# Kernel optimization log

Hardware: AMD Instinct MI355X
Metric: run time of the kernel (lower is better)

## Reference

```python
import jax, jax.numpy as jnp
import numpy as np

WINDOW = 7
NUM_HEADS = 16
HEAD_DIM = 32  # dim=512 / 16 heads
SCALE = HEAD_DIM ** -0.5


def _relative_position_index(ws: int) -> np.ndarray:
    ch, cw = np.meshgrid(np.arange(ws), np.arange(ws), indexing='ij')
    coords = np.stack([ch, cw]).reshape(2, -1)            # [2, ws*ws]
    rel = coords[:, :, None] - coords[:, None, :]          # [2, N, N]
    rel = rel.transpose(1, 2, 0)                           # [N, N, 2]
    rel[:, :, 0] += ws - 1
    rel[:, :, 1] += ws - 1
    rel[:, :, 0] *= 2 * ws - 1
    return rel.sum(-1)                                     # [N, N]

REL_IDX = jnp.asarray(_relative_position_index(WINDOW))   # [49, 49] int


def setup_inputs() -> dict:
    key = jax.random.key(0)
    ks = jax.random.split(key, 6)
    B, N, C = 2048, WINDOW * WINDOW, NUM_HEADS * HEAD_DIM
    return {
        'hidden_states': jax.random.normal(ks[0], (B, N, C), jnp.float32),
        'attention_mask': jnp.zeros((B, N, N), jnp.float32),
        'qkv_w': jax.random.normal(ks[1], (3 * C, C), jnp.float32) * 0.02,
        'qkv_b': jax.random.normal(ks[2], (3 * C,), jnp.float32) * 0.02,
        'out_w': jax.random.normal(ks[3], (C, C), jnp.float32) * 0.02,
        'out_b': jax.random.normal(ks[4], (C,), jnp.float32) * 0.02,
        'rel_pos_table': jax.random.normal(ks[5], ((2 * WINDOW - 1) ** 2, NUM_HEADS), jnp.float32) * 0.02,
    }


def reference(hidden_states, attention_mask, qkv_w, qkv_b, out_w, out_b, rel_pos_table):
    B, N, C = hidden_states.shape
    H, D = NUM_HEADS, HEAD_DIM
    qkv = hidden_states @ qkv_w.T + qkv_b                  # [B, N, 3C]
    q, k, v = jnp.split(qkv, 3, axis=-1)
    q = q.reshape(B, N, H, D).transpose(0, 2, 1, 3)        # [B, H, N, D]
    k = k.reshape(B, N, H, D).transpose(0, 2, 1, 3)
    v = v.reshape(B, N, H, D).transpose(0, 2, 1, 3)
    attn = jnp.einsum('bhnd,bhmd->bhnm', q, k) * SCALE     # [B, H, N, N]
    # relative position bias: gather [N*N] rows -> [N, N, H] -> [1, H, N, N]
    bias = rel_pos_table[REL_IDX.reshape(-1)].reshape(N, N, H).transpose(2, 0, 1)
    attn = attn + bias[None] + attention_mask[:, None]
    attn = jax.nn.softmax(attn, axis=-1)                   # dropout = identity (eval)
    out = jnp.einsum('bhnm,bhmd->bhnd', attn, v)           # [B, H, N, D]
    out = out.transpose(0, 2, 1, 3).reshape(B, N, C)
    return out @ out_w.T + out_b
```

## Files before the change

kernel.cpp:

```cpp
#include <hip/hip_runtime.h>
#include <hip/hip_bf16.h>

typedef __attribute__((ext_vector_type(8))) __bf16 bf16x8;
typedef __attribute__((ext_vector_type(4))) __bf16 bf16x4;
typedef __attribute__((ext_vector_type(4))) float f32x4;

#define MFMA16(a,b,c) __builtin_amdgcn_mfma_f32_16x16x32_bf16(a,b,c,0,0,0)

__device__ __forceinline__ void gload_lds16(const void* g, void* l) {
  __builtin_amdgcn_global_load_lds(
      (const __attribute__((address_space(1))) void*)g,
      (__attribute__((address_space(3))) void*)l, 16, 0, 0);
}

__device__ __forceinline__ f32x4 max4(f32x4 a, f32x4 b) {
  f32x4 c;
  c[0] = fmaxf(a[0], b[0]); c[1] = fmaxf(a[1], b[1]);
  c[2] = fmaxf(a[2], b[2]); c[3] = fmaxf(a[3], b[3]);
  return c;
}

__global__ void prep_k(const float* __restrict__ qkv_w, const float* __restrict__ out_w,
                       const float* __restrict__ rpt,
                       __bf16* __restrict__ qwb, __bf16* __restrict__ owb,
                       __bf16* __restrict__ biasb)
{
  int i = blockIdx.x * 256 + threadIdx.x;
  if (i < 786432) { qwb[i] = (__bf16)qkv_w[i]; return; }
  i -= 786432;
  if (i < 262144) { owb[i] = (__bf16)out_w[i]; return; }
  i -= 262144;
  if (i < 65536) {
    int hh = i >> 12, qc = i & 4095, qq = qc >> 6, c = qc & 63;
    __bf16 val;
    if (c >= 49)      val = (__bf16)(-30000.0f);
    else if (qq >= 49) val = (__bf16)(0.0f);
    else {
      int dh = qq / 7 - c / 7 + 6;
      int dw = qq % 7 - c % 7 + 6;
      val = (__bf16)rpt[(dh * 13 + dw) * 16 + hh];
    }
    biasb[i] = val;
  }
}

__global__ void cast_k(const float* __restrict__ in, __bf16* __restrict__ outb, int n8)
{
  int i = blockIdx.x * blockDim.x + threadIdx.x;
  int stride = gridDim.x * blockDim.x;
  for (; i < n8; i += stride) {
    const float4* p = (const float4*)in + (size_t)i * 2;
    float4 x = p[0], y = p[1];
    bf16x8 o;
    o[0] = (__bf16)x.x; o[1] = (__bf16)x.y; o[2] = (__bf16)x.z; o[3] = (__bf16)x.w;
    o[4] = (__bf16)y.x; o[5] = (__bf16)y.y; o[6] = (__bf16)y.z; o[7] = (__bf16)y.w;
    ((bf16x8*)outb)[i] = o;
  }
}

template<int EPI>
__global__ __launch_bounds__(512, 2)
void gemm8p(const __bf16* __restrict__ A, const __bf16* __restrict__ Bt,
            const float* __restrict__ bvec, float* __restrict__ outp,
            __bf16* __restrict__ qb, __bf16* __restrict__ kb, __bf16* __restrict__ vb,
            int N, int K)
{
  __shared__ __align__(16) char lds[131072];
  const int tid = threadIdx.x;
  const int wave = tid >> 6, lane = tid & 63;
  const int g = lane >> 4, r = lane & 15;
  const int l8 = lane >> 3, l7 = lane & 7;

  const int ntiles = N >> 8;
  const int nper = gridDim.x >> 3;
  const int b2 = (blockIdx.x & 7) * nper + (blockIdx.x >> 3);
  const int m0 = (b2 / ntiles) << 8;
  const int n0 = (b2 % ntiles) << 8;

  const __bf16* Ag = A + (size_t)(m0 + wave * 8 + l8) * K + (l7 ^ l8) * 8;
  const __bf16* Bg = Bt + (size_t)(n0 + wave * 8 + l8) * K + (l7 ^ l8) * 8;
  const size_t c64 = (size_t)64 * K;

  const int ch0 = (g ^ (r & 7)) << 4;
  const int ch1 = ((4 + g) ^ (r & 7)) << 4;
  const char* Ar = lds + ((wave >> 2) * 128 + r) * 128;
  const char* Br = lds + 32768 + ((wave & 3) * 64 + r) * 128;

  f32x4 acc[8][4] = {};
  bf16x8 a[4][2], b[4][2];

#pragma unroll
  for (int c = 0; c < 4; ++c) {
    gload_lds16(Ag + c * c64, lds + wave * 1024 + c * 8192);
    gload_lds16(Bg + c * c64, lds + 32768 + wave * 1024 + c * 8192);
  }
#pragma unroll
  for (int c = 0; c < 4; ++c) {
    gload_lds16(Ag + 64 + c * c64, lds + 65536 + wave * 1024 + c * 8192);
    gload_lds16(Bg + 64 + c * c64, lds + 65536 + 32768 + wave * 1024 + c * 8192);
  }

#pragma unroll 1
  for (int kt = 0; kt < 8; ++kt) {
    const int cur = (kt & 1) << 16;
    const char* Ab = Ar + cur;
    const char* Bb = Br + cur;
    if (kt == 7) asm volatile("s_waitcnt vmcnt(0)" ::: "memory");
    else         asm volatile("s_waitcnt vmcnt(8)" ::: "memory");
    __builtin_amdgcn_s_barrier();

#pragma unroll
    for (int mi = 0; mi < 4; ++mi) {
      a[mi][0] = *(const bf16x8*)(Ab + mi * 2048 + ch0);
      a[mi][1] = *(const bf16x8*)(Ab + mi * 2048 + ch1);
    }
#pragma unroll
    for (int ni = 0; ni < 2; ++ni) {
      b[ni][0] = *(const bf16x8*)(Bb + ni * 2048 + ch0);
      b[ni][1] = *(const bf16x8*)(Bb + ni * 2048 + ch1);
    }
    __builtin_amdgcn_s_barrier();
    asm volatile("s_waitcnt lgkmcnt(0)" ::: "memory");
    __builtin_amdgcn_s_setprio(1);
#pragma unroll
    for (int mi = 0; mi < 4; ++mi)
#pragma unroll
      for (int ni = 0; ni < 2; ++ni) {
        acc[mi][ni] = MFMA16(a[mi][0], b[ni][0], acc[mi][ni]);
        acc[mi][ni] = MFMA16(a[mi][1], b[ni][1], acc[mi][ni]);
      }
    __builtin_amdgcn_s_setprio(0);
    __builtin_amdgcn_s_barrier();

#pragma unroll
    for (int ni = 2; ni < 4; ++ni) {
      b[ni][0] = *(const bf16x8*)(Bb + ni * 2048 + ch0);
      b[ni][1] = *(const bf16x8*)(Bb + ni * 2048 + ch1);
    }
    __builtin_amdgcn_s_barrier();
    asm volatile("s_waitcnt lgkmcnt(0)" ::: "memory");
    __builtin_amdgcn_s_setprio(1);
#pragma unroll
    for (int mi = 0; mi < 4; ++mi)
#pragma unroll
      for (int ni = 2; ni < 4; ++ni) {
        acc[mi][ni] = MFMA16(a[mi][0], b[ni][0], acc[mi][ni]);
        acc[mi][ni] = MFMA16(a[mi][1], b[ni][1], acc[mi][ni]);
      }
    __builtin_amdgcn_s_setprio(0);
    __builtin_amdgcn_s_barrier();

#pragma unroll
    for (int mi = 0; mi < 4; ++mi) {
      a[mi][0] = *(const bf16x8*)(Ab + (4 + mi) * 2048 + ch0);
      a[mi][1] = *(const bf16x8*)(Ab + (4 + mi) * 2048 + ch1);
    }
    __builtin_amdgcn_s_barrier();
    asm volatile("s_waitcnt lgkmcnt(0)" ::: "memory");
    __builtin_amdgcn_s_setprio(1);
#pragma unroll
    for (int mi = 0; mi < 4; ++mi)
#pragma unroll
      for (int ni = 2; ni < 4; ++ni) {
        acc[4 + mi][ni] = MFMA16(a[mi][0], b[ni][0], acc[4 + mi][ni]);
        acc[4 + mi][ni] = MFMA16(a[mi][1], b[ni][1], acc[4 + mi][ni]);
      }
    __builtin_amdgcn_s_setprio(0);
    __builtin_amdgcn_s_barrier();

    if (kt < 6) {
      const __bf16* Agk = Ag + (kt + 2) * 64;
      const __bf16* Bgk = Bg + (kt + 2) * 64;
      char* Al = lds + cur + wave * 1024;
      char* Bl = lds + cur + 32768 + wave * 1024;
#pragma unroll
      for (int c = 0; c < 4; ++c) {
        gload_lds16(Agk + c * c64, Al + c * 8192);
        gload_lds16(Bgk + c * c64, Bl + c * 8192);
      }
    }
    __builtin_amdgcn_s_setprio(1);
#pragma unroll
    for (int mi = 0; mi < 4; ++mi)
#pragma unroll
      for (int ni = 0; ni < 2; ++ni) {
        acc[4 + mi][ni] = MFMA16(a[mi][0], b[ni][0], acc[4 + mi][ni]);
        acc[4 + mi][ni] = MFMA16(a[mi][1], b[ni][1], acc[4 + mi][ni]);
      }
    __builtin_amdgcn_s_setprio(0);
    __builtin_amdgcn_s_barrier();
  }

  if (EPI == 1) {
#pragma unroll
    for (int mi = 0; mi < 8; ++mi) {
      int row = m0 + (wave >> 2) * 128 + mi * 16 + g * 4;
#pragma unroll
      for (int ni = 0; ni < 4; ++ni) {
        int col = n0 + (wave & 3) * 64 + ni * 16 + r;
        float bv = bvec[col];
#pragma unroll
        for (int j = 0; j < 4; ++j)
          outp[(size_t)(row + j) * N + col] = acc[mi][ni][j] + bv;
      }
    }
  } else {
    __bf16* dst; float scl;
    const int which = n0 >> 9;
    if (which == 0)      { dst = qb; scl = 0.17677669529663687f; }
    else if (which == 1) { dst = kb; scl = 1.0f; }
    else                 { dst = vb; scl = 1.0f; }
    float bv[4];
#pragma unroll
    for (int ni = 0; ni < 4; ++ni) bv[ni] = bvec[n0 + (wave & 3) * 64 + ni * 16 + r];
#pragma unroll
    for (int mi = 0; mi < 8; ++mi) {
#pragma unroll
      for (int j = 0; j < 4; ++j) {
        int m = m0 + (wave >> 2) * 128 + mi * 16 + g * 4 + j;
        int bb = m / 49, t = m - bb * 49;
        __bf16* drow = dst + ((size_t)bb * 16) * 1568 + t * 32;
#pragma unroll
        for (int ni = 0; ni < 4; ++ni) {
          int nl = (n0 + (wave & 3) * 64 + ni * 16 + r) & 511;
          int hh = nl >> 5, d = nl & 31;
          float val = (acc[mi][ni][j] + bv[ni]) * scl;
          drow[(size_t)hh * 1568 + d] = (__bf16)val;
        }
      }
    }
  }
}

__global__ __launch_bounds__(256, 4)
void attn_k(const __bf16* __restrict__ qb, const __bf16* __restrict__ kb,
            const __bf16* __restrict__ vb, const __bf16* __restrict__ bias_p,
            const float* __restrict__ mask, __bf16* __restrict__ ao)
{
  __shared__ float maskl[64 * 64];
  __shared__ __bf16 Vt[4][32 * 64];
  __shared__ __bf16 Pl[4][16 * 64];
  const int tid = threadIdx.x, wave = tid >> 6, lane = tid & 63;
  const int g = lane >> 4, r = lane & 15;
  const int b = blockIdx.x >> 2, hg = blockIdx.x & 3;
  const int h = hg * 4 + wave;
  const size_t bh = (size_t)b * 16 + h;
  const __bf16* q = qb + bh * 1568;
  const __bf16* k = kb + bh * 1568;
  const __bf16* v = vb + bh * 1568;
  const bf16x8 z8 = {};
  const f32x4 z4 = {};

  bf16x4 bfr[4][4];
  {
    const __bf16* bp = bias_p + h * 4096;
#pragma unroll
    for (int qi = 0; qi < 4; ++qi)
#pragma unroll
      for (int mi = 0; mi < 4; ++mi)
        bfr[qi][mi] = *(const bf16x4*)(bp + (qi * 16 + r) * 64 + mi * 16 + g * 4);
  }

  bf16x8* vtz = (bf16x8*)Vt[wave];
#pragma unroll
  for (int i = 0; i < 4; ++i) vtz[i * 64 + lane] = z8;

  const float* mb = mask + (size_t)b * 2401;
#pragma unroll
  for (int i = 0; i < 16; ++i) {
    int idx = i * 256 + tid;
    int qq = idx >> 6, c = idx & 63;
    float mv = (qq < 49 && c < 49) ? mb[qq * 49 + c] : 0.0f;
    maskl[qq * 64 + (c ^ ((qq & 7) << 2))] = mv;
  }

  bf16x8 kf[4], qf[4];
#pragma unroll
  for (int i = 0; i < 4; ++i) {
    int row = i * 16 + r;
    kf[i] = (row < 49) ? *(const bf16x8*)(k + row * 32 + g * 8) : z8;
    qf[i] = (row < 49) ? *(const bf16x8*)(q + row * 32 + g * 8) : z8;
  }

  __syncthreads();

  char* vt = (char*)Vt[wave];
#pragma unroll
  for (int i = 0; i < 4; ++i) {
    int idx = i * 64 + lane;
    int t = idx >> 2, d0 = (idx & 3) << 3;
    if (t < 49) {
      bf16x8 vv = *(const bf16x8*)(v + t * 32 + d0);
#pragma unroll
      for (int j = 0; j < 8; ++j) {
        int d = d0 + j;
        *(__bf16*)(vt + d * 128 + ((t * 2) ^ ((d & 7) << 4))) = vv[j];
      }
    }
  }

  bf16x8 vf[2][2];
#pragma unroll
  for (int di = 0; di < 2; ++di) {
    int row = di * 16 + r;
#pragma unroll
    for (int t = 0; t < 2; ++t)
      vf[di][t] = *(const bf16x8*)(vt + row * 128 + (((t * 32 + g * 8) * 2) ^ ((row & 7) << 4)));
  }

  char* pw = (char*)Pl[wave];
  __bf16* aob = ao + (size_t)b * 25088 + h * 32;
  const int swz = (r & 7) << 4;
  const int mswz = (r & 7) << 2;

#pragma unroll
  for (int qi = 0; qi < 4; ++qi) {
    f32x4 s[4];
#pragma unroll
    for (int mi = 0; mi < 4; ++mi) s[mi] = MFMA16(kf[mi], qf[qi], z4);

    const int qrow = qi * 16 + r;
#pragma unroll
    for (int mi = 0; mi < 4; ++mi) {
      int c0 = mi * 16 + g * 4;
      f32x4 m4 = *(const f32x4*)(maskl + qrow * 64 + (c0 ^ mswz));
#pragma unroll
      for (int jj = 0; jj < 4; ++jj)
        s[mi][jj] += (float)bfr[qi][mi][jj] + m4[jj];
    }
    f32x4 aa = max4(max4(s[0], s[1]), max4(s[2], s[3]));
    float mx = fmaxf(fmaxf(aa[0], aa[1]), fmaxf(aa[2], aa[3]));
    mx = fmaxf(mx, __shfl_xor(mx, 16));
    mx = fmaxf(mx, __shfl_xor(mx, 32));
    float sum = 0.0f;
#pragma unroll
    for (int mi = 0; mi < 4; ++mi) {
#pragma unroll
      for (int jj = 0; jj < 4; ++jj) {
        float e = __expf(s[mi][jj] - mx);
        s[mi][jj] = e;
        sum += e;
      }
    }
    sum += __shfl_xor(sum, 16);
    sum += __shfl_xor(sum, 32);
    const float rinv = 1.0f / sum;

#pragma unroll
    for (int mi = 0; mi < 4; ++mi) {
      bf16x4 w;
#pragma unroll
      for (int jj = 0; jj < 4; ++jj) w[jj] = (__bf16)(s[mi][jj] * rinv);
      *(bf16x4*)(pw + r * 128 + (((mi * 16 + g * 4) * 2) ^ swz)) = w;
    }
    bf16x8 pa0 = *(const bf16x8*)(pw + r * 128 + ((g * 16) ^ swz));
    bf16x8 pa1 = *(const bf16x8*)(pw + r * 128 + ((64 + g * 16) ^ swz));

#pragma unroll
    for (int di = 0; di < 2; ++di) {
      f32x4 o = MFMA16(pa0, vf[di][0], z4);
      o = MFMA16(pa1, vf[di][1], o);
#pragma unroll
      for (int jj = 0; jj < 4; ++jj) {
        int qq = qi * 16 + g * 4 + jj;
        if (qq < 49)
          aob[(size_t)qq * 512 + di * 16 + r] = (__bf16)o[jj];
      }
    }
  }
}

extern "C" void kernel_launch(void* const* d_in, const int* in_sizes, int n_in,
                              void* d_out, int out_size, void* d_ws, size_t ws_size,
                              hipStream_t stream)
{
  const float* hs    = (const float*)d_in[0];
  const float* mask  = (const float*)d_in[1];
  const float* qkv_w = (const float*)d_in[2];
  const float* qkv_b = (const float*)d_in[3];
  const float* out_w = (const float*)d_in[4];
  const float* out_b = (const float*)d_in[5];
  const float* rpt   = (const float*)d_in[6];
  float* out = (float*)d_out;

  char* ws = (char*)d_ws;
  __bf16* hsb  = (__bf16*)(ws);
  __bf16* qb   = (__bf16*)(ws + 102760448);
  __bf16* kb   = (__bf16*)(ws + 205520896);
  __bf16* vb   = (__bf16*)(ws + 308281344);
  __bf16* qwb  = (__bf16*)(ws + 411041792);
  __bf16* owb  = (__bf16*)(ws + 412614656);
  __bf16* biasb= (__bf16*)(ws + 413138944);

  prep_k<<<4352, 256, 0, stream>>>(qkv_w, out_w, rpt, qwb, owb, biasb);
  cast_k<<<2048, 256, 0, stream>>>(hs, hsb, 6422528);
  gemm8p<0><<<2352, 512, 0, stream>>>(hsb, qwb, qkv_b, nullptr, qb, kb, vb,
                                      1536, 512);
  attn_k<<<8192, 256, 0, stream>>>(qb, kb, vb, biasb, mask, hsb);
  gemm8p<1><<<784, 512, 0, stream>>>(hsb, owb, out_b, out, nullptr, nullptr, nullptr,
                                     512, 512);
}
```

Before: 540.2 us.

## Fuse fp32-to-bf16 input cast into QKV GEMM A-tile loading

Removes the separate cast kernel and instead has the QKV GEMM load fp32 hidden states through registers, convert them to bf16, and write them swizzled into LDS, while B still uses direct global-to-LDS loads. This avoids writing and re-reading an intermediate bf16 copy of the activations. In exchange, the GEMM reads twice the bytes for A on every N-tile and uses synchronous vmcnt(0) waits that may weaken the load/compute overlap. The attention kernel also now loads bias fragments inside the loop instead of holding them all in registers, which lowers register pressure.

Result: slower. 555.4 us (+2.8%).

```diff
diff --git a/kernel.cpp b/kernel.cpp
--- a/kernel.cpp
+++ b/kernel.cpp
@@ -44,23 +44,9 @@
   }
 }
 
-__global__ void cast_k(const float* __restrict__ in, __bf16* __restrict__ outb, int n8)
-{
-  int i = blockIdx.x * blockDim.x + threadIdx.x;
-  int stride = gridDim.x * blockDim.x;
-  for (; i < n8; i += stride) {
-    const float4* p = (const float4*)in + (size_t)i * 2;
-    float4 x = p[0], y = p[1];
-    bf16x8 o;
-    o[0] = (__bf16)x.x; o[1] = (__bf16)x.y; o[2] = (__bf16)x.z; o[3] = (__bf16)x.w;
-    o[4] = (__bf16)y.x; o[5] = (__bf16)y.y; o[6] = (__bf16)y.z; o[7] = (__bf16)y.w;
-    ((bf16x8*)outb)[i] = o;
-  }
-}
-
-template<int EPI>
+template<int EPI, int CVT>
 __global__ __launch_bounds__(512, 2)
-void gemm8p(const __bf16* __restrict__ A, const __bf16* __restrict__ Bt,
+void gemm8p(const void* __restrict__ Aptr, const __bf16* __restrict__ Bt,
             const float* __restrict__ bvec, float* __restrict__ outp,
             __bf16* __restrict__ qb, __bf16* __restrict__ kb, __bf16* __restrict__ vb,
             int N, int K)
@@ -77,9 +63,14 @@
   const int m0 = (b2 / ntiles) << 8;
   const int n0 = (b2 % ntiles) << 8;
 
-  const __bf16* Ag = A + (size_t)(m0 + wave * 8 + l8) * K + (l7 ^ l8) * 8;
+  const __bf16* Ab16 = (const __bf16*)Aptr;
+  const float*  Af32 = (const float*)Aptr;
+  const __bf16* Ag = Ab16 + (size_t)(m0 + wave * 8 + l8) * K + (l7 ^ l8) * 8;
   const __bf16* Bg = Bt + (size_t)(n0 + wave * 8 + l8) * K + (l7 ^ l8) * 8;
   const size_t c64 = (size_t)64 * K;
+
+  const int rowg = tid >> 4, q = tid & 15;
+  f32x4 aF[8];
 
   const int ch0 = (g ^ (r & 7)) << 4;
   const int ch1 = ((4 + g) ^ (r & 7)) << 4;
@@ -89,15 +80,44 @@
   f32x4 acc[8][4] = {};
   bf16x8 a[4][2], b[4][2];
 
-#pragma unroll
-  for (int c = 0; c < 4; ++c) {
-    gload_lds16(Ag + c * c64, lds + wave * 1024 + c * 8192);
-    gload_lds16(Bg + c * c64, lds + 32768 + wave * 1024 + c * 8192);
-  }
-#pragma unroll
-  for (int c = 0; c < 4; ++c) {
-    gload_lds16(Ag + 64 + c * c64, lds + 65536 + wave * 1024 + c * 8192);
-    gload_lds16(Bg + 64 + c * c64, lds + 65536 + 32768 + wave * 1024 + c * 8192);
+#define STAGEB_(T) {                                                           \
+    const __bf16* Bs_ = Bg + (T) * 64;                                         \
+    char* Bl_ = lds + (((T) & 1) << 16) + 32768 + wave * 1024;                 \
+    _Pragma("unroll")                                                          \
+    for (int c = 0; c < 4; ++c) gload_lds16(Bs_ + c * c64, Bl_ + c * 8192); }
+#define LOADA_F32_(T) {                                                        \
+    _Pragma("unroll")                                                          \
+    for (int j = 0; j < 8; ++j) {                                              \
+      int row_ = rowg + j * 32;                                                \
+      aF[j] = *(const f32x4*)(Af32 + (size_t)(m0 + row_) * 512 + (T) * 64 + q * 4); } }
+#define WRITEA_(T) {                                                           \
+    char* dA_ = lds + (((T) & 1) << 16);                                       \
+    _Pragma("unroll")                                                          \
+    for (int j = 0; j < 8; ++j) {                                              \
+      int row_ = rowg + j * 32;                                                \
+      bf16x4 w_;                                                               \
+      w_[0] = (__bf16)aF[j][0]; w_[1] = (__bf16)aF[j][1];                      \
+      w_[2] = (__bf16)aF[j][2]; w_[3] = (__bf16)aF[j][3];                      \
+      *(bf16x4*)(dA_ + row_ * 128 + (((q >> 1) ^ (row_ & 7)) << 4) + ((q & 1) << 3)) = w_; } }
+
+  if (CVT) {
+    STAGEB_(0); STAGEB_(1);
+    LOADA_F32_(0);
+    asm volatile("s_waitcnt vmcnt(0)" ::: "memory");
+    WRITEA_(0);
+    LOADA_F32_(1);
+    asm volatile("s_waitcnt lgkmcnt(0)" ::: "memory");
+  } else {
+#pragma unroll
+    for (int c = 0; c < 4; ++c) {
+      gload_lds16(Ag + c * c64, lds + wave * 1024 + c * 8192);
+      gload_lds16(Bg + c * c64, lds + 32768 + wave * 1024 + c * 8192);
+    }
+#pragma unroll
+    for (int c = 0; c < 4; ++c) {
+      gload_lds16(Ag + 64 + c * c64, lds + 65536 + wave * 1024 + c * 8192);
+      gload_lds16(Bg + 64 + c * c64, lds + 65536 + 32768 + wave * 1024 + c * 8192);
+    }
   }
 
 #pragma unroll 1
@@ -105,8 +125,10 @@
     const int cur = (kt & 1) << 16;
     const char* Ab = Ar + cur;
     const char* Bb = Br + cur;
-    if (kt == 7) asm volatile("s_waitcnt vmcnt(0)" ::: "memory");
-    else         asm volatile("s_waitcnt vmcnt(8)" ::: "memory");
+    if (!CVT) {
+      if (kt == 7) asm volatile("s_waitcnt vmcnt(0)" ::: "memory");
+      else         asm volatile("s_waitcnt vmcnt(8)" ::: "memory");
+    }
     __builtin_amdgcn_s_barrier();
 
 #pragma unroll
@@ -119,6 +141,7 @@
       b[ni][0] = *(const bf16x8*)(Bb + ni * 2048 + ch0);
       b[ni][1] = *(const bf16x8*)(Bb + ni * 2048 + ch1);
     }
+    if (CVT && kt >= 1 && kt < 7) LOADA_F32_(kt + 1);
     __builtin_amdgcn_s_barrier();
     asm volatile("s_waitcnt lgkmcnt(0)" ::: "memory");
     __builtin_amdgcn_s_setprio(1);
@@ -168,15 +191,23 @@
     __builtin_amdgcn_s_setprio(0);
     __builtin_amdgcn_s_barrier();
 
-    if (kt < 6) {
-      const __bf16* Agk = Ag + (kt + 2) * 64;
-      const __bf16* Bgk = Bg + (kt + 2) * 64;
-      char* Al = lds + cur + wave * 1024;
-      char* Bl = lds + cur + 32768 + wave * 1024;
-#pragma unroll
-      for (int c = 0; c < 4; ++c) {
-        gload_lds16(Agk + c * c64, Al + c * 8192);
-        gload_lds16(Bgk + c * c64, Bl + c * 8192);
+    if (CVT) {
+      if (kt < 7) {
+        asm volatile("s_waitcnt vmcnt(0)" ::: "memory");
+        WRITEA_(kt + 1);
+      }
+      if (kt < 6) STAGEB_(kt + 2);
+    } else {
+      if (kt < 6) {
+        const __bf16* Agk = Ag + (kt + 2) * 64;
+        const __bf16* Bgk = Bg + (kt + 2) * 64;
+        char* Al = lds + cur + wave * 1024;
+        char* Bl = lds + cur + 32768 + wave * 1024;
+#pragma unroll
+        for (int c = 0; c < 4; ++c) {
+          gload_lds16(Agk + c * c64, Al + c * 8192);
+          gload_lds16(Bgk + c * c64, Bl + c * 8192);
+        }
       }
     }
     __builtin_amdgcn_s_setprio(1);
@@ -188,8 +219,12 @@
         acc[4 + mi][ni] = MFMA16(a[mi][1], b[ni][1], acc[4 + mi][ni]);
       }
     __builtin_amdgcn_s_setprio(0);
-    __builtin_amdgcn_s_barrier();
-  }
+    if (CVT) asm volatile("s_waitcnt lgkmcnt(0)" ::: "memory");
+    __builtin_amdgcn_s_barrier();
+  }
+#undef STAGEB_
+#undef LOADA_F32_
+#undef WRITEA_
 
   if (EPI == 1) {
 #pragma unroll
@@ -251,16 +286,6 @@
   const bf16x8 z8 = {};
   const f32x4 z4 = {};
 
-  bf16x4 bfr[4][4];
-  {
-    const __bf16* bp = bias_p + h * 4096;
-#pragma unroll
-    for (int qi = 0; qi < 4; ++qi)
-#pragma unroll
-      for (int mi = 0; mi < 4; ++mi)
-        bfr[qi][mi] = *(const bf16x4*)(bp + (qi * 16 + r) * 64 + mi * 16 + g * 4);
-  }
-
   bf16x8* vtz = (bf16x8*)Vt[wave];
 #pragma unroll
   for (int i = 0; i < 4; ++i) vtz[i * 64 + lane] = z8;
@@ -308,6 +333,7 @@
       vf[di][t] = *(const bf16x8*)(vt + row * 128 + (((t * 32 + g * 8) * 2) ^ ((row & 7) << 4)));
   }
 
+  const __bf16* bp = bias_p + h * 4096;
   char* pw = (char*)Pl[wave];
   __bf16* aob = ao + (size_t)b * 25088 + h * 32;
   const int swz = (r & 7) << 4;
@@ -323,10 +349,11 @@
 #pragma unroll
     for (int mi = 0; mi < 4; ++mi) {
       int c0 = mi * 16 + g * 4;
+      bf16x4 b4 = *(const bf16x4*)(bp + qrow * 64 + c0);
       f32x4 m4 = *(const f32x4*)(maskl + qrow * 64 + (c0 ^ mswz));
 #pragma unroll
       for (int jj = 0; jj < 4; ++jj)
-        s[mi][jj] += (float)bfr[qi][mi][jj] + m4[jj];
+        s[mi][jj] += (float)b4[jj] + m4[jj];
     }
     f32x4 aa = max4(max4(s[0], s[1]), max4(s[2], s[3]));
     float mx = fmaxf(fmaxf(aa[0], aa[1]), fmaxf(aa[2], aa[3]));
@@ -384,7 +411,7 @@
   float* out = (float*)d_out;
 
   char* ws = (char*)d_ws;
-  __bf16* hsb  = (__bf16*)(ws);
+  __bf16* aob  = (__bf16*)(ws);
   __bf16* qb   = (__bf16*)(ws + 102760448);
   __bf16* kb   = (__bf16*)(ws + 205520896);
   __bf16* vb   = (__bf16*)(ws + 308281344);
@@ -393,10 +420,9 @@
   __bf16* biasb= (__bf16*)(ws + 413138944);
 
   prep_k<<<4352, 256, 0, stream>>>(qkv_w, out_w, rpt, qwb, owb, biasb);
-  cast_k<<<2048, 256, 0, stream>>>(hs, hsb, 6422528);
-  gemm8p<0><<<2352, 512, 0, stream>>>(hsb, qwb, qkv_b, nullptr, qb, kb, vb,
-                                      1536, 512);
-  attn_k<<<8192, 256, 0, stream>>>(qb, kb, vb, biasb, mask, hsb);
-  gemm8p<1><<<784, 512, 0, stream>>>(hsb, owb, out_b, out, nullptr, nullptr, nullptr,
-                                     512, 512);
-}
+  gemm8p<0, 1><<<2352, 512, 0, stream>>>(hs, qwb, qkv_b, nullptr, qb, kb, vb,
+                                         1536, 512);
+  attn_k<<<8192, 256, 0, stream>>>(qb, kb, vb, biasb, mask, aob);
+  gemm8p<1, 0><<<784, 512, 0, stream>>>(aob, owb, out_b, out, nullptr, nullptr, nullptr,
+                                        512, 512);
+}
```
